# Optimization experiments

Hardware: AMD Instinct MI355X
Metric: run time of the kernel (lower is better)

The kernel has to match this reference:

```python
import jax, jax.numpy as jnp
import numpy as np

ALPHA1 = 0.1
ALPHA2 = 0.1
NOISE = 0.02
B, T, H, O = 128, 512, 512, 3


def setup_inputs() -> dict:
    key = jax.random.key(0)
    ks = jax.random.split(key, 10)
    return {
        "x": jax.random.normal(ks[0], (B, T, 5), dtype=jnp.float32),
        "wi_stim": jax.random.normal(ks[1], (3, H), dtype=jnp.float32) / np.sqrt(3),
        "wrec11": jax.random.normal(ks[2], (H, H), dtype=jnp.float32) / np.sqrt(H),
        "wi_ctx": jax.random.normal(ks[3], (2, H), dtype=jnp.float32) / np.sqrt(2),
        "wrec22": jax.random.normal(ks[4], (H, H), dtype=jnp.float32) / np.sqrt(H),
        "wrec12": jax.random.normal(ks[5], (H, H), dtype=jnp.float32) / np.sqrt(H),
        "wrec21": jax.random.normal(ks[6], (H, H), dtype=jnp.float32) / np.sqrt(H),
        "wo": jax.random.normal(ks[7], (H, O), dtype=jnp.float32) / np.sqrt(H),
        "noise1": jax.random.normal(ks[8], (T, B, H), dtype=jnp.float32),
        "noise2": jax.random.normal(ks[9], (T, B, H), dtype=jnp.float32),
    }


def reference(x, wi_stim, wrec11, wi_ctx, wrec22, wrec12, wrec21, wo, noise1, noise2):
    # x: [B, T, 5]; noise: [T, B, H] (pre-sampled standard normals, scaled by NOISE)
    xs = jnp.transpose(x[:, :, :3], (1, 0, 2))  # [T, B, 3]
    xc = jnp.transpose(x[:, :, 3:], (1, 0, 2))  # [T, B, 2]

    def step(carry, inp):
        h1, h2 = carry
        xsi, xci, n1, n2 = inp
        h1 = (1 - ALPHA1) * h1 + ALPHA1 * (
            xsi @ wi_stim + jnp.tanh(h1) @ wrec11 + jnp.tanh(h2) @ wrec12 + n1 * NOISE
        )
        # note: h2 update uses the freshly-updated h1 (as in the torch loop)
        h2 = (1 - ALPHA2) * h2 + ALPHA2 * (
            xci @ wi_ctx + jnp.tanh(h1) @ wrec21 + jnp.tanh(h2) @ wrec22 + n2 * NOISE
        )
        return (h1, h2), jnp.tanh(h2) @ wo

    h0 = jnp.zeros((x.shape[0], wrec11.shape[0]), dtype=x.dtype)
    _, out_t = jax.lax.scan(step, (h0, h0), (xs, xc, noise1, noise2))  # [T, B, O]
    return jnp.transpose(out_t, (1, 0, 2))  # [B, T, O]
```

## Files before the change

kernel.cpp:

```cpp
#include <hip/hip_runtime.h>
#include <hip/hip_bf16.h>

#define TT 512
#define BB 128
#define HH 512
#define NGROUP 8
#define NSLICE 8
#define ALPHA 0.1f
#define NOISE_S 0.02f

typedef __attribute__((ext_vector_type(8))) short short8;
typedef __attribute__((ext_vector_type(8))) _Float16 half8;
typedef __attribute__((ext_vector_type(4))) float f32x4;

#define WPACK_CH 132096
#define PUB1_B (WPACK_CH * 16)
#define PUB2_B (PUB1_B + NGROUP * 32768)

__device__ __forceinline__ unsigned short f2h(float f) {
  return __builtin_bit_cast(unsigned short, (_Float16)f);
}

__device__ __forceinline__ float fast_tanh(float x) {
  float e = __builtin_amdgcn_exp2f(x * 2.8853900817779268f);
  return 1.0f - 2.0f * __builtin_amdgcn_rcpf(e + 1.0f);
}

__device__ __forceinline__ f32x4 mfma16(short8 a, short8 b, f32x4 c) {
  return __builtin_amdgcn_mfma_f32_16x16x32_f16(
      __builtin_bit_cast(half8, a), __builtin_bit_cast(half8, b), c, 0, 0, 0);
}

__global__ void pack_weights(const float* __restrict__ w11, const float* __restrict__ w12,
                             const float* __restrict__ w21, const float* __restrict__ w22,
                             const float* __restrict__ wo, unsigned short* __restrict__ dst) {
  int idx = blockIdx.x * 256 + threadIdx.x;
  if (idx < 131072) {
    int which = idx >> 16;
    int c0 = idx & 65535;
    int kt = c0 >> 11, rem = c0 & 2047;
    int nt = rem >> 6, lane = rem & 63;
    const float* wlo = which ? w21 : w11;
    const float* whi = which ? w22 : w12;
    unsigned short* p = dst + (size_t)idx * 8;
    int n = nt * 16 + (lane & 15);
    int kb = kt * 32 + ((lane >> 4) & 3) * 8;
#pragma unroll
    for (int i = 0; i < 8; ++i) {
      int k = kb + i;
      float v = (k < HH) ? wlo[k * HH + n] : whi[(k - HH) * HH + n];
      p[i] = f2h(v);
    }
  } else if (idx < 132096) {
    int c0 = idx - 131072;
    int kt = c0 >> 6, lane = c0 & 63;
    unsigned short* p = dst + (size_t)131072 * 8 + (size_t)c0 * 8;
    int n = lane & 15;
    int kb = kt * 32 + ((lane >> 4) & 3) * 8;
#pragma unroll
    for (int i = 0; i < 8; ++i) {
      float v = (n < 3) ? wo[(kb + i) * 3 + n] : 0.0f;
      p[i] = f2h(v);
    }
  }
}

__global__ void zero_ws(int* __restrict__ p, int n) {
  for (int i = blockIdx.x * 256 + threadIdx.x; i < n; i += gridDim.x * 256)
    p[i] = 0;
}

__global__ __launch_bounds__(256, 1)
void rnn_main(const float* __restrict__ x, const float* __restrict__ wi_stim,
              const float* __restrict__ wi_ctx, const float* __restrict__ noise1,
              const float* __restrict__ noise2, char* __restrict__ ws,
              float* __restrict__ out) {
  __shared__ __align__(16) unsigned short T1buf[16 * 512];
  __shared__ __align__(16) unsigned short T2buf[16 * 512];
  __shared__ __align__(16) unsigned short WOlds[16 * 512];
  __shared__ float xstage[2][16][5];

  const int tid = threadIdx.x;
  const int w = tid >> 6, lane = tid & 63;
  const int c16 = lane & 15, kh = lane >> 4;
  const int g = blockIdx.x & (NGROUP - 1);
  const int slice = blockIdx.x >> 3;
  const int nt = slice * 4 + w;
  const int n0 = nt * 16;
  const int b0 = g * 16;
  const int lrow0 = kh * 4;

  const short8* __restrict__ WC = (const short8*)ws;
  unsigned* __restrict__ pub1 = (unsigned*)(ws + PUB1_B) + g * 8192;
  unsigned* __restrict__ pub2 = (unsigned*)(ws + PUB2_B) + g * 8192;

  short8 z = {0, 0, 0, 0, 0, 0, 0, 0};
  for (int i = tid; i < 1024; i += 256) {
    ((short8*)T1buf)[i] = z;
    ((short8*)T2buf)[i] = z;
  }
#pragma unroll
  for (int c = 0; c < 4; ++c) {
    int kt = w * 4 + c;
    short8 v = WC[131072 + kt * 64 + lane];
    *(short8*)&WOlds[kt * 512 + lane * 8] = v;
  }
  if (tid < 80) {
    int b = tid / 5, c = tid % 5;
    xstage[0][b][c] = x[((size_t)(b0 + b) * TT + 0) * 5 + c];
  }

  short8 wA[32], wB[32];
#pragma unroll
  for (int kt = 0; kt < 32; ++kt) {
    wA[kt] = WC[kt * 2048 + nt * 64 + lane];
    wB[kt] = WC[65536 + kt * 2048 + nt * 64 + lane];
  }
#pragma unroll
  for (int kt = 0; kt < 32; ++kt) {
    asm volatile("" : "+v"(wA[kt]));
    asm volatile("" : "+v"(wB[kt]));
  }

  float wis[3], wic[2];
#pragma unroll
  for (int c = 0; c < 3; ++c) wis[c] = wi_stim[c * HH + n0 + c16];
#pragma unroll
  for (int c = 0; c < 2; ++c) wic[c] = wi_ctx[c * HH + n0 + c16];

  float h1[4] = {0, 0, 0, 0}, h2[4] = {0, 0, 0, 0};

  const int kt_p = nt >> 1;
  const int hi = (((nt & 1) * 16) + c16) >> 3;
  const int ci = c16 & 7;

  auto stage_poll = [&](const unsigned* pubw, unsigned short* Tbuf, unsigned exp) {
    unsigned long long v[4][4];
    bool ok;
    do {
      ok = true;
#pragma unroll
      for (int c = 0; c < 4; ++c) {
        const unsigned long long* src =
            (const unsigned long long*)(pubw + ((w * 4 + c) << 9)) + lane * 4;
#pragma unroll
        for (int j = 0; j < 4; ++j) {
          v[c][j] = __hip_atomic_load(&src[j], __ATOMIC_RELAXED,
                                      __HIP_MEMORY_SCOPE_AGENT);
          ok &= (((unsigned)(v[c][j] >> 16) & 0xffffu) >= exp);
          ok &= ((unsigned)(v[c][j] >> 48) >= exp);
        }
      }
    } while (!ok);
    __builtin_amdgcn_sched_barrier(0);
    asm volatile("" ::: "memory");
#pragma unroll
    for (int c = 0; c < 4; ++c) {
      unsigned long long u0 = (v[c][0] & 0xffffull)
                            | (((v[c][0] >> 32) & 0xffffull) << 16)
                            | ((v[c][1] & 0xffffull) << 32)
                            | (((v[c][1] >> 32) & 0xffffull) << 48);
      unsigned long long u1 = (v[c][2] & 0xffffull)
                            | (((v[c][2] >> 32) & 0xffffull) << 16)
                            | ((v[c][3] & 0xffffull) << 32)
                            | (((v[c][3] >> 32) & 0xffffull) << 48);
      *(unsigned long long*)&Tbuf[(w * 4 + c) * 512 + lane * 8] = u0;
      *(unsigned long long*)&Tbuf[(w * 4 + c) * 512 + lane * 8 + 4] = u1;
    }
  };

  __syncthreads();

  for (int t = 0; t < TT; ++t) {
    const int buf = t & 1;
    const unsigned tagA = (unsigned)(t + 1) << 16;

    float n1v[4];
#pragma unroll
    for (int r = 0; r < 4; ++r)
      n1v[r] = noise1[((size_t)t * BB + b0 + lrow0 + r) * HH + n0 + c16];

    f32x4 aA = {0, 0, 0, 0}, aB = {0, 0, 0, 0};
#pragma unroll
    for (int kt = 0; kt < 16; ++kt) {
      short8 a1 = *(const short8*)&T1buf[kt * 512 + lane * 8];
      aA = mfma16(a1, wA[kt], aA);
    }
    stage_poll(pub2, T2buf, (unsigned)t);
    __syncthreads();
#pragma unroll
    for (int kt = 0; kt < 16; ++kt) {
      short8 a2 = *(const short8*)&T2buf[kt * 512 + lane * 8];
      aB = mfma16(a2, wA[16 + kt], aB);
    }

    if (t > 0 && slice == ((t - 1) & 7) && w == 0) {
      f32x4 ao = {0, 0, 0, 0};
#pragma unroll
      for (int kt = 0; kt < 16; ++kt) {
        short8 a2 = *(const short8*)&T2buf[kt * 512 + lane * 8];
        short8 bo = *(const short8*)&WOlds[kt * 512 + lane * 8];
        ao = mfma16(a2, bo, ao);
      }
      if (c16 < 3) {
#pragma unroll
        for (int r = 0; r < 4; ++r)
          out[((size_t)(b0 + lrow0 + r) * TT + (t - 1)) * 3 + c16] = ao[r];
      }
    }

    unsigned short tp[4];
#pragma unroll
    for (int r = 0; r < 4; ++r) {
      float pre = aA[r] + aB[r]
                + wis[0] * xstage[buf][lrow0 + r][0]
                + wis[1] * xstage[buf][lrow0 + r][1]
                + wis[2] * xstage[buf][lrow0 + r][2]
                + NOISE_S * n1v[r];
      float h = (1.0f - ALPHA) * h1[r] + ALPHA * pre;
      h1[r] = h;
      tp[r] = f2h(fast_tanh(h));
    }
#pragma unroll
    for (int r = 0; r < 4; ++r)
      __hip_atomic_store(&pub1[kt_p * 512 + (lrow0 + r + hi * 16) * 8 + ci],
                         tagA | tp[r], __ATOMIC_RELAXED, __HIP_MEMORY_SCOPE_AGENT);

    float n2v[4];
#pragma unroll
    for (int r = 0; r < 4; ++r)
      n2v[r] = noise2[((size_t)t * BB + b0 + lrow0 + r) * HH + n0 + c16];

    f32x4 bA = {0, 0, 0, 0}, bB = {0, 0, 0, 0};
#pragma unroll
    for (int kt = 0; kt < 16; ++kt) {
      short8 a2 = *(const short8*)&T2buf[kt * 512 + lane * 8];
      bB = mfma16(a2, wB[16 + kt], bB);
    }
    stage_poll(pub1, T1buf, (unsigned)(t + 1));
    if (t + 1 < TT && tid < 80) {
      int b = tid / 5, c = tid % 5;
      xstage[buf ^ 1][b][c] = x[((size_t)(b0 + b) * TT + (t + 1)) * 5 + c];
    }
    __syncthreads();
#pragma unroll
    for (int kt = 0; kt < 16; ++kt) {
      short8 a1 = *(const short8*)&T1buf[kt * 512 + lane * 8];
      bA = mfma16(a1, wB[kt], bA);
    }
#pragma unroll
    for (int r = 0; r < 4; ++r) {
      float pre = bA[r] + bB[r]
                + wic[0] * xstage[buf][lrow0 + r][3]
                + wic[1] * xstage[buf][lrow0 + r][4]
                + NOISE_S * n2v[r];
      float h = (1.0f - ALPHA) * h2[r] + ALPHA * pre;
      h2[r] = h;
      tp[r] = f2h(fast_tanh(h));
    }
#pragma unroll
    for (int r = 0; r < 4; ++r)
      __hip_atomic_store(&pub2[kt_p * 512 + (lrow0 + r + hi * 16) * 8 + ci],
                         tagA | tp[r], __ATOMIC_RELAXED, __HIP_MEMORY_SCOPE_AGENT);
  }

  if (slice == ((TT - 1) & 7)) {
    stage_poll(pub2, T2buf, (unsigned)TT);
    __syncthreads();
    if (w == 0) {
      f32x4 ao = {0, 0, 0, 0};
#pragma unroll
      for (int kt = 0; kt < 16; ++kt) {
        short8 a2 = *(const short8*)&T2buf[kt * 512 + lane * 8];
        short8 bo = *(const short8*)&WOlds[kt * 512 + lane * 8];
        ao = mfma16(a2, bo, ao);
      }
      if (c16 < 3) {
#pragma unroll
        for (int r = 0; r < 4; ++r)
          out[((size_t)(b0 + lrow0 + r) * TT + (TT - 1)) * 3 + c16] = ao[r];
      }
    }
  }
}

extern "C" void kernel_launch(void* const* d_in, const int* in_sizes, int n_in,
                              void* d_out, int out_size, void* d_ws, size_t ws_size,
                              hipStream_t stream) {
  const float* x       = (const float*)d_in[0];
  const float* wi_stim = (const float*)d_in[1];
  const float* w11     = (const float*)d_in[2];
  const float* wi_ctx  = (const float*)d_in[3];
  const float* w22     = (const float*)d_in[4];
  const float* w12     = (const float*)d_in[5];
  const float* w21     = (const float*)d_in[6];
  const float* wo      = (const float*)d_in[7];
  const float* n1      = (const float*)d_in[8];
  const float* n2      = (const float*)d_in[9];
  char* ws = (char*)d_ws;

  int nz = (NGROUP * 32768 * 2) / 4;
  zero_ws<<<64, 256, 0, stream>>>((int*)(ws + PUB1_B), nz);
  pack_weights<<<516, 256, 0, stream>>>(w11, w12, w21, w22, wo,
                                        (unsigned short*)ws);
  rnn_main<<<NSLICE * NGROUP, 256, 0, stream>>>(x, wi_stim, wi_ctx, n1, n2, ws,
                                                (float*)d_out);
}
```

Measured before the change: 3.578 ms.

## Stage own tanh slice in LDS, publish coalesced, stream weights from global

Each block now writes its own tanh outputs straight into its local T buffers and skips polling its own slice. After a barrier it publishes those values with coalesced 64-bit tagged stores instead of scattered 32-bit atomics. The recurrent weights are no longer held in 64 short8 registers; they are read from global memory (and cache) on every MFMA. This frees many VGPRs and cuts redundant polling, but adds extra __syncthreads and per-step global weight traffic on the critical recurrence path.

```diff
diff --git a/kernel.cpp b/kernel.cpp
--- a/kernel.cpp
+++ b/kernel.cpp
@@ -110,18 +110,6 @@
     xstage[0][b][c] = x[((size_t)(b0 + b) * TT + 0) * 5 + c];
   }
 
-  short8 wA[32], wB[32];
-#pragma unroll
-  for (int kt = 0; kt < 32; ++kt) {
-    wA[kt] = WC[kt * 2048 + nt * 64 + lane];
-    wB[kt] = WC[65536 + kt * 2048 + nt * 64 + lane];
-  }
-#pragma unroll
-  for (int kt = 0; kt < 32; ++kt) {
-    asm volatile("" : "+v"(wA[kt]));
-    asm volatile("" : "+v"(wB[kt]));
-  }
-
   float wis[3], wic[2];
 #pragma unroll
   for (int c = 0; c < 3; ++c) wis[c] = wi_stim[c * HH + n0 + c16];
@@ -133,16 +121,36 @@
   const int kt_p = nt >> 1;
   const int hi = (((nt & 1) * 16) + c16) >> 3;
   const int ci = c16 & 7;
+  const int lslot = kt_p * 512 + (lrow0 + hi * 16) * 8 + ci;
+
+  const int pbase = slice * 1024 + tid * 4;
+
+  const short8* __restrict__ WAp = WC + nt * 64 + lane;
+  const short8* __restrict__ WBp = WC + 65536 + nt * 64 + lane;
+
+  auto publish_own = [&](const unsigned short* Tbuf, unsigned* pubw, unsigned tagN) {
+    unsigned long long lv = *(const unsigned long long*)&Tbuf[pbase];
+    unsigned w0 = tagN | (unsigned)(lv & 0xffffull);
+    unsigned w1 = tagN | (unsigned)((lv >> 16) & 0xffffull);
+    unsigned w2 = tagN | (unsigned)((lv >> 32) & 0xffffull);
+    unsigned w3 = tagN | (unsigned)((lv >> 48) & 0xffffull);
+    unsigned long long p0 = (unsigned long long)w0 | ((unsigned long long)w1 << 32);
+    unsigned long long p1 = (unsigned long long)w2 | ((unsigned long long)w3 << 32);
+    unsigned long long* dst = (unsigned long long*)&pubw[pbase];
+    __hip_atomic_store(&dst[0], p0, __ATOMIC_RELAXED, __HIP_MEMORY_SCOPE_AGENT);
+    __hip_atomic_store(&dst[1], p1, __ATOMIC_RELAXED, __HIP_MEMORY_SCOPE_AGENT);
+  };
 
   auto stage_poll = [&](const unsigned* pubw, unsigned short* Tbuf, unsigned exp) {
     unsigned long long v[4][4];
-    bool ok;
-    do {
-      ok = true;
+    for (;;) {
+      bool ok = true;
 #pragma unroll
       for (int c = 0; c < 4; ++c) {
+        int kt = w * 4 + c;
+        if ((kt >> 1) == slice) continue;
         const unsigned long long* src =
-            (const unsigned long long*)(pubw + ((w * 4 + c) << 9)) + lane * 4;
+            (const unsigned long long*)(pubw + (kt << 9)) + lane * 4;
 #pragma unroll
         for (int j = 0; j < 4; ++j) {
           v[c][j] = __hip_atomic_load(&src[j], __ATOMIC_RELAXED,
@@ -151,11 +159,14 @@
           ok &= ((unsigned)(v[c][j] >> 48) >= exp);
         }
       }
-    } while (!ok);
+      if (ok) break;
+    }
     __builtin_amdgcn_sched_barrier(0);
     asm volatile("" ::: "memory");
 #pragma unroll
     for (int c = 0; c < 4; ++c) {
+      int kt = w * 4 + c;
+      if ((kt >> 1) == slice) continue;
       unsigned long long u0 = (v[c][0] & 0xffffull)
                             | (((v[c][0] >> 32) & 0xffffull) << 16)
                             | ((v[c][1] & 0xffffull) << 32)
@@ -164,8 +175,8 @@
                             | (((v[c][2] >> 32) & 0xffffull) << 16)
                             | ((v[c][3] & 0xffffull) << 32)
                             | (((v[c][3] >> 32) & 0xffffull) << 48);
-      *(unsigned long long*)&Tbuf[(w * 4 + c) * 512 + lane * 8] = u0;
-      *(unsigned long long*)&Tbuf[(w * 4 + c) * 512 + lane * 8 + 4] = u1;
+      *(unsigned long long*)&Tbuf[kt * 512 + lane * 8] = u0;
+      *(unsigned long long*)&Tbuf[kt * 512 + lane * 8 + 4] = u1;
     }
   };
 
@@ -173,25 +184,28 @@
 
   for (int t = 0; t < TT; ++t) {
     const int buf = t & 1;
-    const unsigned tagA = (unsigned)(t + 1) << 16;
-
-    float n1v[4];
-#pragma unroll
-    for (int r = 0; r < 4; ++r)
-      n1v[r] = noise1[((size_t)t * BB + b0 + lrow0 + r) * HH + n0 + c16];
+    const unsigned tagN = (unsigned)(t + 1) << 16;
+
+    float n1v[4], n2v[4];
+#pragma unroll
+    for (int r = 0; r < 4; ++r) {
+      size_t rowoff = ((size_t)t * BB + b0 + lrow0 + r) * HH + n0 + c16;
+      n1v[r] = noise1[rowoff];
+      n2v[r] = noise2[rowoff];
+    }
 
     f32x4 aA = {0, 0, 0, 0}, aB = {0, 0, 0, 0};
 #pragma unroll
     for (int kt = 0; kt < 16; ++kt) {
       short8 a1 = *(const short8*)&T1buf[kt * 512 + lane * 8];
-      aA = mfma16(a1, wA[kt], aA);
+      aA = mfma16(a1, WAp[kt * 2048], aA);
     }
     stage_poll(pub2, T2buf, (unsigned)t);
     __syncthreads();
 #pragma unroll
     for (int kt = 0; kt < 16; ++kt) {
       short8 a2 = *(const short8*)&T2buf[kt * 512 + lane * 8];
-      aB = mfma16(a2, wA[16 + kt], aB);
+      aB = mfma16(a2, WAp[(16 + kt) * 2048], aB);
     }
 
     if (t > 0 && slice == ((t - 1) & 7) && w == 0) {
@@ -209,7 +223,6 @@
       }
     }
 
-    unsigned short tp[4];
 #pragma unroll
     for (int r = 0; r < 4; ++r) {
       float pre = aA[r] + aB[r]
@@ -219,23 +232,16 @@
                 + NOISE_S * n1v[r];
       float h = (1.0f - ALPHA) * h1[r] + ALPHA * pre;
       h1[r] = h;
-      tp[r] = f2h(fast_tanh(h));
-    }
-#pragma unroll
-    for (int r = 0; r < 4; ++r)
-      __hip_atomic_store(&pub1[kt_p * 512 + (lrow0 + r + hi * 16) * 8 + ci],
-                         tagA | tp[r], __ATOMIC_RELAXED, __HIP_MEMORY_SCOPE_AGENT);
-
-    float n2v[4];
-#pragma unroll
-    for (int r = 0; r < 4; ++r)
-      n2v[r] = noise2[((size_t)t * BB + b0 + lrow0 + r) * HH + n0 + c16];
+      T1buf[lslot + r * 8] = f2h(fast_tanh(h));
+    }
+    __syncthreads();
+    publish_own(T1buf, pub1, tagN);
 
     f32x4 bA = {0, 0, 0, 0}, bB = {0, 0, 0, 0};
 #pragma unroll
     for (int kt = 0; kt < 16; ++kt) {
       short8 a2 = *(const short8*)&T2buf[kt * 512 + lane * 8];
-      bB = mfma16(a2, wB[16 + kt], bB);
+      bB = mfma16(a2, WBp[(16 + kt) * 2048], bB);
     }
     stage_poll(pub1, T1buf, (unsigned)(t + 1));
     if (t + 1 < TT && tid < 80) {
@@ -246,7 +252,7 @@
 #pragma unroll
     for (int kt = 0; kt < 16; ++kt) {
       short8 a1 = *(const short8*)&T1buf[kt * 512 + lane * 8];
-      bA = mfma16(a1, wB[kt], bA);
+      bA = mfma16(a1, WBp[kt * 2048], bA);
     }
 #pragma unroll
     for (int r = 0; r < 4; ++r) {
@@ -256,12 +262,10 @@
                 + NOISE_S * n2v[r];
       float h = (1.0f - ALPHA) * h2[r] + ALPHA * pre;
       h2[r] = h;
-      tp[r] = f2h(fast_tanh(h));
-    }
-#pragma unroll
-    for (int r = 0; r < 4; ++r)
-      __hip_atomic_store(&pub2[kt_p * 512 + (lrow0 + r + hi * 16) * 8 + ci],
-                         tagA | tp[r], __ATOMIC_RELAXED, __HIP_MEMORY_SCOPE_AGENT);
+      T2buf[lslot + r * 8] = f2h(fast_tanh(h));
+    }
+    __syncthreads();
+    publish_own(T2buf, pub2, tagN);
   }
 
   if (slice == ((TT - 1) & 7)) {
```

New measurement: 4.300 ms. 1.2x slower.
